# Performance work log

Measured on AMD Instinct MI355X. Metric: run time of the kernel, lower is better.

## Reference

```python
import jax, jax.numpy as jnp
import numpy as np

H, DH, BS, NSEL, WIN = 16, 64, 4, 4, 32  # heads, dim_head, compress/selection block, top-k blocks, sliding window


def rmsnorm(x):
    return x * jax.lax.rsqrt(jnp.mean(x * x, axis=-1, keepdims=True) + 1e-6)


def rope(x):
    # x: [B,S,H,d]; standard rotate-half RoPE, theta=10000
    B, S, Hh, d = x.shape
    half = d // 2
    inv = 1.0 / (10000.0 ** (jnp.arange(half, dtype=jnp.float32) / half))
    t = jnp.arange(S, dtype=jnp.float32)[:, None] * inv[None, :]
    cos = jnp.cos(t)[None, :, None, :]
    sin = jnp.sin(t)[None, :, None, :]
    x1, x2 = x[..., :half], x[..., half:]
    return jnp.concatenate([x1 * cos - x2 * sin, x1 * sin + x2 * cos], axis=-1)


def setup_inputs() -> dict:
    key = jax.random.key(0)
    ks = jax.random.split(key, 20)
    B, S, D = 2, 1024, 1024
    s = 0.02
    f32 = jnp.float32
    return {
        'x': jax.random.normal(ks[0], (B, S, D), f32),
        've': jax.random.normal(ks[1], (B, S, D), f32),
        'x0': jax.random.normal(ks[2], (B, S, D), f32),
        'lambdas': jnp.array([1.0, 0.0], f32),
        'Wq': jax.random.normal(ks[3], (D, H * DH), f32) * s,
        'Wk': jax.random.normal(ks[4], (D, H * DH), f32) * s,
        'Wv': jax.random.normal(ks[5], (D, H * DH), f32) * s,
        'pos_k': jax.random.normal(ks[6], (H, BS, DH), f32) * s,
        'pos_v': jax.random.normal(ks[7], (H, BS, DH), f32) * s,
        'Wck': jax.random.normal(ks[8], (BS * DH, DH), f32) * s,
        'Wcv': jax.random.normal(ks[9], (BS * DH, DH), f32) * s,
        'mem_k': jax.random.normal(ks[10], (H, 1, DH), f32) * s,
        'mem_v': jax.random.normal(ks[11], (H, 1, DH), f32) * s,
        'Wg': jax.random.normal(ks[12], (D, 3 * H), f32) * s,
        'Wo': jax.random.normal(ks[13], (H * DH, D), f32) * s,
        'Wfc': jax.random.normal(ks[14], (D, 4 * D), f32) * s,
        'Wproj': jax.random.normal(ks[15], (4 * D, D), f32) * s,
    }


def nsa_block(x, ve, x0, lambdas, Wq, Wk, Wv, pos_k, pos_v, Wck, Wcv, mem_k, mem_v, Wg, Wo, Wfc, Wproj):
    B, S, D = x.shape
    nB = S // BS
    scale = DH ** -0.5
    pos = jnp.arange(S)

    # lambda residual blend + rmsnorm (ve unused by NSA block)
    xr = lambdas[0] * x + lambdas[1] * x0
    h = rmsnorm(xr)

    q = (h @ Wq).reshape(B, S, H, DH)
    k = (h @ Wk).reshape(B, S, H, DH)
    v = (h @ Wv).reshape(B, S, H, DH)

    # ---- compressed-block branch ----
    kb = k.reshape(B, nB, BS, H, DH) + pos_k.transpose(1, 0, 2)[None, None]
    vb = v.reshape(B, nB, BS, H, DH) + pos_v.transpose(1, 0, 2)[None, None]
    kc = kb.transpose(0, 1, 3, 2, 4).reshape(B, nB, H, BS * DH) @ Wck  # [B,nB,H,d]
    vc = vb.transpose(0, 1, 3, 2, 4).reshape(B, nB, H, BS * DH) @ Wcv
    kc = jnp.concatenate([jnp.broadcast_to(mem_k.transpose(1, 0, 2)[None], (B, 1, H, DH)), kc], axis=1)
    vc = jnp.concatenate([jnp.broadcast_to(mem_v.transpose(1, 0, 2)[None], (B, 1, H, DH)), vc], axis=1)
    cs = jnp.einsum('bshd,bnhd->bhsn', q, kc) * scale
    block_last = jnp.arange(nB) * BS + (BS - 1)
    cvis = jnp.concatenate([jnp.ones((S, 1), bool), block_last[None, :] <= pos[:, None]], axis=1)
    cp = jax.nn.softmax(jnp.where(cvis[None, None], cs, -jnp.inf), axis=-1)
    cout = jnp.einsum('bhsn,bnhd->bshd', cp, vc)

    # ---- fine selected-block branch (top-k blocks by compressed attn mass + own diagonal block) ----
    imp = cp[..., 1:]  # [B,H,S,nB], zero for blocks not fully in the past
    sel_val, sel_idx = jax.lax.top_k(imp, NSEL)
    own = jnp.broadcast_to((pos // BS)[None, None, :, None], (B, H, S, 1)).astype(sel_idx.dtype)
    idx_all = jnp.concatenate([sel_idx, own], axis=-1)  # [B,H,S,NSEL+1]

    qr, kr = rope(q), rope(k)
    krb = kr.reshape(B, nB, BS, H, DH).transpose(0, 3, 1, 2, 4)  # [B,H,nB,Bs,d]
    vrb = v.reshape(B, nB, BS, H, DH).transpose(0, 3, 1, 2, 4)
    M = NSEL + 1
    idxf = idx_all.reshape(B, H, S * M, 1, 1)
    gk = jnp.take_along_axis(krb, idxf, axis=2).reshape(B, H, S, M * BS, DH)
    gv = jnp.take_along_axis(vrb, idxf, axis=2).reshape(B, H, S, M * BS, DH)
    kpos = idx_all[..., None] * BS + jnp.arange(BS)  # [B,H,S,M,Bs]
    vblock = jnp.concatenate([sel_val > 0, jnp.ones((B, H, S, 1), bool)], axis=-1)
    fmask = (vblock[..., None] & (kpos <= pos[None, None, :, None, None])).reshape(B, H, S, M * BS)
    fs = jnp.einsum('bshd,bhsmd->bhsm', qr, gk) * scale
    fp = jax.nn.softmax(jnp.where(fmask, fs, -jnp.inf), axis=-1)
    fout = jnp.einsum('bhsm,bhsmd->bshd', fp, gv)

    # ---- sliding-window branch ----
    off = jnp.arange(WIN)
    spos = pos[:, None] - off[None, :]  # [S,W]
    idx_s = jnp.clip(spos, 0, S - 1)
    ks_ = kr[:, idx_s]  # [B,S,W,H,d]
    vs_ = v[:, idx_s]
    ss = jnp.einsum('bshd,bswhd->bhsw', qr, ks_) * scale
    sp = jax.nn.softmax(jnp.where((spos >= 0)[None, None], ss, -jnp.inf), axis=-1)
    sout = jnp.einsum('bhsw,bswhd->bshd', sp, vs_)

    # ---- gated combine + out proj + MLP (relu^2) ----
    g = jax.nn.sigmoid(h @ Wg).reshape(B, S, H, 3)
    o = g[..., 0:1] * cout + g[..., 1:2] * fout + g[..., 2:3] * sout
    x1 = xr + o.reshape(B, S, H * DH) @ Wo
    m = rmsnorm(x1)
    return x1 + (jax.nn.relu(m @ Wfc) ** 2) @ Wproj


def reference(x, ve, x0, lambdas, Wq, Wk, Wv, pos_k, pos_v, Wck, Wcv, mem_k, mem_v, Wg, Wo, Wfc, Wproj):
    return nsa_block(x, ve, x0, lambdas, Wq, Wk, Wv, pos_k, pos_v, Wck, Wcv, mem_k, mem_v, Wg, Wo, Wfc, Wproj)
```

## Files before the change

### kernel.cpp

```cpp
#include <hip/hip_runtime.h>

constexpr int cH = 16, cDH = 64, cBS = 4, cNSEL = 4, cWIN = 32;
constexpr int cB = 2, cS = 1024, cD = 1024;
constexpr int cNB = 256, cNBLK = 257, cDFF = 4096, cM = 2048;
constexpr float cSCALE = 0.125f;
constexpr int cSSTR = 258;
constexpr int cNP = 288;

typedef unsigned short u16;
typedef unsigned int u32;
typedef __attribute__((ext_vector_type(8))) __bf16 bf16x8;
typedef __attribute__((ext_vector_type(8))) u16 u16x8;
typedef __attribute__((ext_vector_type(4))) float f32x4;
static_assert(sizeof(bf16x8) == 16, "bf16x8 must be 16B");

__device__ __forceinline__ float sigf(float x) { return 1.f / (1.f + expf(-x)); }
__device__ __forceinline__ float b2f(u16 u) {
  union { float f; u32 u; } c; c.u = ((u32)u) << 16; return c.f;
}
__device__ __forceinline__ u16 f2b(float f) {
  union { float f; u32 u; } c; c.f = f;
  u32 u = c.u;
  return (u16)((u + 0x7fffu + ((u >> 16) & 1u)) >> 16);
}
__device__ __forceinline__ void split_bf(float v, u16& h, u16& l) {
  h = f2b(v);
  l = f2b(v - b2f(h));
}

typedef const __attribute__((address_space(1))) void* gas_t;
typedef __attribute__((address_space(3))) void* las_t;
__device__ __forceinline__ void gload16(void* lds, const void* g) {
  __builtin_amdgcn_global_load_lds((gas_t)g, (las_t)lds, 16, 0, 0);
}

__global__ __launch_bounds__(256) void k_fill(float* __restrict__ p, float v)
{
  p[blockIdx.x * 256 + threadIdx.x] = v;
}

__global__ __launch_bounds__(256) void k_lerp_rmsnorm(
    const float* __restrict__ x, const float* __restrict__ x0,
    const float* __restrict__ lambdas, float* __restrict__ xr, float* __restrict__ h,
    u16* __restrict__ hbh, u16* __restrict__ hbl)
{
  int row = blockIdx.x, tid = threadIdx.x;
  float l0 = lambdas[0], l1 = lambdas[1];
  size_t base = (size_t)row * cD + tid * 4;
  float4 xa = *(const float4*)(x + base);
  float4 xb = *(const float4*)(x0 + base);
  float v0 = l0 * xa.x + l1 * xb.x;
  float v1 = l0 * xa.y + l1 * xb.y;
  float v2 = l0 * xa.z + l1 * xb.z;
  float v3 = l0 * xa.w + l1 * xb.w;
  float ss = v0*v0 + v1*v1 + v2*v2 + v3*v3;
  #pragma unroll
  for (int o = 32; o; o >>= 1) ss += __shfl_xor(ss, o);
  __shared__ float red[4];
  if ((tid & 63) == 0) red[tid >> 6] = ss;
  __syncthreads();
  float tot = red[0] + red[1] + red[2] + red[3];
  float sc = rsqrtf(tot * (1.0f / cD) + 1e-6f);
  *(float4*)(xr + base) = make_float4(v0, v1, v2, v3);
  float h0 = v0*sc, h1 = v1*sc, h2 = v2*sc, h3 = v3*sc;
  *(float4*)(h + base) = make_float4(h0, h1, h2, h3);
  if (hbh) {
    ushort4 hv, lv;
    split_bf(h0, hv.x, lv.x); split_bf(h1, hv.y, lv.y);
    split_bf(h2, hv.z, lv.z); split_bf(h3, hv.w, lv.w);
    *(ushort4*)(hbh + base) = hv;
    *(ushort4*)(hbl + base) = lv;
  }
}

__global__ __launch_bounds__(256) void k_rmsnorm(
    const float* __restrict__ x, float* __restrict__ out,
    u16* __restrict__ obh, u16* __restrict__ obl)
{
  int row = blockIdx.x, tid = threadIdx.x;
  size_t base = (size_t)row * cD + tid * 4;
  float4 v = *(const float4*)(x + base);
  float ss = v.x*v.x + v.y*v.y + v.z*v.z + v.w*v.w;
  #pragma unroll
  for (int o = 32; o; o >>= 1) ss += __shfl_xor(ss, o);
  __shared__ float red[4];
  if ((tid & 63) == 0) red[tid >> 6] = ss;
  __syncthreads();
  float tot = red[0] + red[1] + red[2] + red[3];
  float sc = rsqrtf(tot * (1.0f / cD) + 1e-6f);
  float h0 = v.x*sc, h1 = v.y*sc, h2 = v.z*sc, h3 = v.w*sc;
  if (out) *(float4*)(out + base) = make_float4(h0, h1, h2, h3);
  if (obh) {
    ushort4 hv, lv;
    split_bf(h0, hv.x, lv.x); split_bf(h1, hv.y, lv.y);
    split_bf(h2, hv.z, lv.z); split_bf(h3, hv.w, lv.w);
    *(ushort4*)(obh + base) = hv;
    *(ushort4*)(obl + base) = lv;
  }
}

template<int EPI>
__global__ __launch_bounds__(256) void k_gemm(
    const float* __restrict__ A, const float* __restrict__ Bw,
    const float* __restrict__ R, float* __restrict__ C, int M, int N, int K)
{
  constexpr int BM = 64, BN = 64, BK = 16;
  __shared__ float As[BK][BM];
  __shared__ float Bs[BK][BN];
  int tid = threadIdx.x;
  int tx = tid & 15, ty = tid >> 4;
  int m0 = blockIdx.y * BM, n0 = blockIdx.x * BN;
  float acc[4][4] = {};
  for (int k0 = 0; k0 < K; k0 += BK) {
    {
      int r = tid >> 2, c4 = (tid & 3) << 2;
      float4 av = *(const float4*)(A + (size_t)(m0 + r) * K + k0 + c4);
      As[c4+0][r] = av.x; As[c4+1][r] = av.y; As[c4+2][r] = av.z; As[c4+3][r] = av.w;
    }
    {
      int kr = tid >> 4, c4 = (tid & 15) << 2;
      int n = n0 + c4;
      const float* bp = Bw + (size_t)(k0 + kr) * N;
      if (n + 3 < N) {
        float4 bv = *(const float4*)(bp + n);
        Bs[kr][c4+0] = bv.x; Bs[kr][c4+1] = bv.y; Bs[kr][c4+2] = bv.z; Bs[kr][c4+3] = bv.w;
      } else {
        #pragma unroll
        for (int j = 0; j < 4; j++) Bs[kr][c4+j] = (n + j < N) ? bp[n + j] : 0.f;
      }
    }
    __syncthreads();
    #pragma unroll
    for (int kk = 0; kk < BK; ++kk) {
      float4 a4 = *(const float4*)&As[kk][ty << 2];
      float4 b4 = *(const float4*)&Bs[kk][tx << 2];
      float av[4] = {a4.x, a4.y, a4.z, a4.w};
      float bv[4] = {b4.x, b4.y, b4.z, b4.w};
      #pragma unroll
      for (int i = 0; i < 4; i++)
        #pragma unroll
        for (int j = 0; j < 4; j++) acc[i][j] += av[i] * bv[j];
    }
    __syncthreads();
  }
  #pragma unroll
  for (int i = 0; i < 4; i++) {
    int m = m0 + (ty << 2) + i;
    #pragma unroll
    for (int j = 0; j < 4; j++) {
      int n = n0 + (tx << 2) + j;
      if (n < N) {
        float vv = acc[i][j];
        if (EPI == 1) vv = vv > 0.f ? vv * vv : 0.f;
        if (R) vv += R[(size_t)m * N + n];
        C[(size_t)m * N + n] = vv;
      }
    }
  }
}

__global__ __launch_bounds__(256) void k_wsplit_t(
    const float* __restrict__ W, u16* __restrict__ Th, u16* __restrict__ Tl, int K, int N)
{
  __shared__ float tile[32][33];
  int n0 = blockIdx.x * 32, k0 = blockIdx.y * 32;
  int r = threadIdx.x >> 3, c4 = (threadIdx.x & 7) << 2;
  float4 v = *(const float4*)(W + (size_t)(k0 + r) * N + n0 + c4);
  tile[r][c4+0] = v.x; tile[r][c4+1] = v.y; tile[r][c4+2] = v.z; tile[r][c4+3] = v.w;
  __syncthreads();
  float f0 = tile[c4+0][r], f1 = tile[c4+1][r], f2 = tile[c4+2][r], f3 = tile[c4+3][r];
  ushort4 hv, lv;
  split_bf(f0, hv.x, lv.x); split_bf(f1, hv.y, lv.y);
  split_bf(f2, hv.z, lv.z); split_bf(f3, hv.w, lv.w);
  size_t ob = (size_t)(n0 + r) * K + k0 + c4;
  *(ushort4*)(Th + ob) = hv;
  *(ushort4*)(Tl + ob) = lv;
}

__global__ __launch_bounds__(256) void k_wsplit_g(
    const float* __restrict__ W, u16* __restrict__ Th, u16* __restrict__ Tl)
{
  int idx = blockIdx.x * 256 + threadIdx.x;
  int n = idx >> 10, kk = idx & 1023;
  float v = (n < 48) ? W[(size_t)kk * 48 + n] : 0.f;
  u16 hb, lb; split_bf(v, hb, lb);
  Th[idx] = hb; Tl[idx] = lb;
}

template<int BM, int BN, int EPI, int OUTBF, int TERMS>
__global__ __launch_bounds__(256) void k_mfma_gemm(
    const u16* __restrict__ Ah_g, const u16* __restrict__ Al_g,
    const u16* __restrict__ Bh_g, const u16* __restrict__ Bl_g,
    const float* __restrict__ R, float* __restrict__ Cf,
    u16* __restrict__ Ch, u16* __restrict__ Cl,
    int M, int N, int K)
{
  constexpr int BK = 64;
  constexpr int MR = BM / 32, NR = BN / 32;
  __shared__ u16 lds[(BM + BN) * BK * 2];
  u16* Ah = lds;
  u16* Al = Ah + BM * BK;
  u16* Bh = Al + BM * BK;
  u16* Bl = Bh + BN * BK;

  int tid = threadIdx.x;
  int lane = tid & 63, wave = tid >> 6;
  int wr = wave >> 1, wc = wave & 1;
  int l16 = lane & 15, rg = lane >> 4;

  int nwg = gridDim.x * gridDim.y;
  int lin = blockIdx.y * gridDim.x + blockIdx.x;
  if ((nwg & 7) == 0) lin = (lin & 7) * (nwg >> 3) + (lin >> 3);
  int m0 = (lin / gridDim.x) * BM, n0 = (lin % gridDim.x) * BN;

  f32x4 acc[MR][NR];
  #pragma unroll
  for (int m = 0; m < MR; m++)
    #pragma unroll
    for (int n = 0; n < NR; n++) acc[m][n] = (f32x4){0.f, 0.f, 0.f, 0.f};

  for (int k0 = 0; k0 < K; k0 += BK) {
    #pragma unroll
    for (int c = tid; c < BM * 8; c += 256) {
      int row = c >> 3, gs = (c & 7) ^ (row & 7);
      size_t off = (size_t)(m0 + row) * K + k0 + (gs << 3);
      gload16(Ah + c * 8, Ah_g + off);
      gload16(Al + c * 8, Al_g + off);
    }
    #pragma unroll
    for (int c = tid; c < BN * 8; c += 256) {
      int row = c >> 3, gs = (c & 7) ^ (row & 7);
      size_t off = (size_t)(n0 + row) * K + k0 + (gs << 3);
      gload16(Bh + c * 8, Bh_g + off);
      gload16(Bl + c * 8, Bl_g + off);
    }
    __syncthreads();

    #pragma unroll
    for (int ks = 0; ks < 2; ks++) {
      bf16x8 ah[MR], al[MR];
      #pragma unroll
      for (int m = 0; m < MR; m++) {
        int r = wr * (BM / 2) + m * 16 + l16;
        int sl = ((ks << 2) + rg) ^ (r & 7);
        ah[m] = *(const bf16x8*)&Ah[r * BK + (sl << 3)];
        al[m] = *(const bf16x8*)&Al[r * BK + (sl << 3)];
      }
      #pragma unroll
      for (int n = 0; n < NR; n++) {
        int r = wc * (BN / 2) + n * 16 + l16;
        int sl = ((ks << 2) + rg) ^ (r & 7);
        bf16x8 bh = *(const bf16x8*)&Bh[r * BK + (sl << 3)];
        bf16x8 bl = *(const bf16x8*)&Bl[r * BK + (sl << 3)];
        #pragma unroll
        for (int m = 0; m < MR; m++) {
          acc[m][n] = __builtin_amdgcn_mfma_f32_16x16x32_bf16(ah[m], bh, acc[m][n], 0, 0, 0);
          acc[m][n] = __builtin_amdgcn_mfma_f32_16x16x32_bf16(ah[m], bl, acc[m][n], 0, 0, 0);
          acc[m][n] = __builtin_amdgcn_mfma_f32_16x16x32_bf16(al[m], bh, acc[m][n], 0, 0, 0);
          if (TERMS == 4)
            acc[m][n] = __builtin_amdgcn_mfma_f32_16x16x32_bf16(al[m], bl, acc[m][n], 0, 0, 0);
        }
      }
    }
    __syncthreads();
  }

  int rbase = m0 + wr * (BM / 2) + (rg << 2);
  #pragma unroll
  for (int m = 0; m < MR; m++) {
    #pragma unroll
    for (int j = 0; j < 4; j++) {
      int row = rbase + m * 16 + j;
      #pragma unroll
      for (int n = 0; n < NR; n++) {
        int col = n0 + wc * (BN / 2) + n * 16 + l16;
        float v = acc[m][n][j];
        if (EPI == 1) v = v > 0.f ? v * v : 0.f;
        if (R) v += R[(size_t)row * N + col];
        if (OUTBF != 1) Cf[(size_t)row * N + col] = v;
        if (OUTBF >= 1) {
          u16 hb, lb; split_bf(v, hb, lb);
          Ch[(size_t)row * N + col] = hb;
          Cl[(size_t)row * N + col] = lb;
        }
      }
    }
  }
}

__global__ __launch_bounds__(256) void k_mfma_qkvg(
    const u16* __restrict__ Ahg, const u16* __restrict__ Alg,
    const u16* __restrict__ BqH, const u16* __restrict__ BqL,
    const u16* __restrict__ BkH, const u16* __restrict__ BkL,
    const u16* __restrict__ BvH, const u16* __restrict__ BvL,
    const u16* __restrict__ BgH, const u16* __restrict__ BgL,
    float* __restrict__ qo, float* __restrict__ ko, float* __restrict__ vo,
    float* __restrict__ gpre, u16* __restrict__ qbh, u16* __restrict__ qbl)
{
  constexpr int BM = 64, BN = 64, BK = 64, K = cD;
  __shared__ u16 lds[(BM + BN) * BK * 2];
  u16* Ah = lds;
  u16* Al = Ah + BM * BK;
  u16* Bh = Al + BM * BK;
  u16* Bl = Bh + BN * BK;

  int tid = threadIdx.x;
  int lane = tid & 63, wave = tid >> 6;
  int wr = wave >> 1, wc = wave & 1;
  int l16 = lane & 15, rg = lane >> 4;

  int nwg = gridDim.x * gridDim.y;
  int lin = blockIdx.y * gridDim.x + blockIdx.x;
  lin = (lin & 7) * (nwg >> 3) + (lin >> 3);
  int bx = lin % gridDim.x, by = lin / gridDim.x;
  int mat = bx >> 4;
  int n0 = (bx - (mat << 4)) * BN;
  int m0 = by * BM;

  const u16* Bh_g; const u16* Bl_g;
  if (mat == 0)      { Bh_g = BqH; Bl_g = BqL; }
  else if (mat == 1) { Bh_g = BkH; Bl_g = BkL; }
  else if (mat == 2) { Bh_g = BvH; Bl_g = BvL; }
  else               { Bh_g = BgH; Bl_g = BgL; }

  f32x4 acc[2][2];
  #pragma unroll
  for (int m = 0; m < 2; m++)
    #pragma unroll
    for (int n = 0; n < 2; n++) acc[m][n] = (f32x4){0.f, 0.f, 0.f, 0.f};

  for (int k0 = 0; k0 < K; k0 += BK) {
    #pragma unroll
    for (int c = tid; c < BM * 8; c += 256) {
      int row = c >> 3, gs = (c & 7) ^ (row & 7);
      size_t off = (size_t)(m0 + row) * K + k0 + (gs << 3);
      gload16(Ah + c * 8, Ahg + off);
      gload16(Al + c * 8, Alg + off);
    }
    #pragma unroll
    for (int c = tid; c < BN * 8; c += 256) {
      int row = c >> 3, gs = (c & 7) ^ (row & 7);
      size_t off = (size_t)(n0 + row) * K + k0 + (gs << 3);
      gload16(Bh + c * 8, Bh_g + off);
      gload16(Bl + c * 8, Bl_g + off);
    }
    __syncthreads();

    #pragma unroll
    for (int ks = 0; ks < 2; ks++) {
      bf16x8 ah[2], al[2];
      #pragma unroll
      for (int m = 0; m < 2; m++) {
        int r = wr * 32 + m * 16 + l16;
        int sl = ((ks << 2) + rg) ^ (r & 7);
        ah[m] = *(const bf16x8*)&Ah[r * BK + (sl << 3)];
        al[m] = *(const bf16x8*)&Al[r * BK + (sl << 3)];
      }
      #pragma unroll
      for (int n = 0; n < 2; n++) {
        int r = wc * 32 + n * 16 + l16;
        int sl = ((ks << 2) + rg) ^ (r & 7);
        bf16x8 bh = *(const bf16x8*)&Bh[r * BK + (sl << 3)];
        bf16x8 bl = *(const bf16x8*)&Bl[r * BK + (sl << 3)];
        #pragma unroll
        for (int m = 0; m < 2; m++) {
          acc[m][n] = __builtin_amdgcn_mfma_f32_16x16x32_bf16(ah[m], bh, acc[m][n], 0, 0, 0);
          acc[m][n] = __builtin_amdgcn_mfma_f32_16x16x32_bf16(ah[m], bl, acc[m][n], 0, 0, 0);
          acc[m][n] = __builtin_amdgcn_mfma_f32_16x16x32_bf16(al[m], bh, acc[m][n], 0, 0, 0);
          acc[m][n] = __builtin_amdgcn_mfma_f32_16x16x32_bf16(al[m], bl, acc[m][n], 0, 0, 0);
        }
      }
    }
    __syncthreads();
  }

  int rbase = m0 + wr * 32 + (rg << 2);
  #pragma unroll
  for (int m = 0; m < 2; m++) {
    #pragma unroll
    for (int j = 0; j < 4; j++) {
      int row = rbase + m * 16 + j;
      #pragma unroll
      for (int n = 0; n < 2; n++) {
        int col = n0 + wc * 32 + n * 16 + l16;
        float v = acc[m][n][j];
        if (mat == 0) {
          qo[(size_t)row * cD + col] = v;
          u16 hb, lb; split_bf(v, hb, lb);
          qbh[(size_t)row * cD + col] = hb;
          qbl[(size_t)row * cD + col] = lb;
        } else if (mat == 1) {
          ko[(size_t)row * cD + col] = v;
        } else if (mat == 2) {
          vo[(size_t)row * cD + col] = v;
        } else if (col < 48) {
          gpre[(size_t)row * 48 + col] = v;
        }
      }
    }
  }
}

__global__ __launch_bounds__(64) void k_compress4(
    const float* __restrict__ kbuf, const float* __restrict__ vbuf,
    const float* __restrict__ pos_k, const float* __restrict__ pos_v,
    const float* __restrict__ Wck, const float* __restrict__ Wcv,
    const float* __restrict__ mem_k, const float* __restrict__ mem_v,
    float* __restrict__ kc, float* __restrict__ vc)
{
  int idx = blockIdx.x;
  int h = idx % cH; int n = (idx / cH) % cNBLK; int b = idx / (cH * cNBLK);
  int d = threadIdx.x;
  size_t co = (((size_t)b * cNBLK + n) * cH + h) * cDH + d;
  if (n == 0) {
    kc[co] = mem_k[h * cDH + d];
    vc[co] = mem_v[h * cDH + d];
    return;
  }
  __shared__ float kb[cBS * cDH], vb[cBS * cDH];
  int nb = n - 1;
  for (int t = d; t < cBS * cDH; t += 64) {
    int i = t >> 6, e = t & 63;
    size_t src = (((size_t)b * cS + nb * cBS + i) * cH + h) * cDH + e;
    kb[t] = kbuf[src] + pos_k[(h * cBS + i) * cDH + e];
    vb[t] = vbuf[src] + pos_v[(h * cBS + i) * cDH + e];
  }
  __syncthreads();
  float ak = 0.f, av = 0.f;
  #pragma unroll 4
  for (int j = 0; j < cBS * cDH; ++j) {
    ak += kb[j] * Wck[(size_t)j * cDH + d];
    av += vb[j] * Wcv[(size_t)j * cDH + d];
  }
  kc[co] = ak; vc[co] = av;
}

__global__ __launch_bounds__(256) void k_compress4_bf(
    const float* __restrict__ kbuf, const float* __restrict__ vbuf,
    const float* __restrict__ pos_k, const float* __restrict__ pos_v,
    const float* __restrict__ Wck, const float* __restrict__ Wcv,
    const float* __restrict__ mem_k, const float* __restrict__ mem_v,
    u16* __restrict__ kch, u16* __restrict__ kcl,
    u16* __restrict__ vth, u16* __restrict__ vtl)
{
  int wave = threadIdx.x >> 6, d = threadIdx.x & 63;
  int idx = blockIdx.x * 4 + wave;
  int h = idx % cH;
  int n = (idx / cH) % cNBLK;
  int b = idx / (cH * cNBLK);
  float ak, av;
  if (n == 0) {
    ak = mem_k[h * cDH + d];
    av = mem_v[h * cDH + d];
    size_t vr = ((size_t)(b * cH + h) * cDH + d) * cNP;
    for (int p = cNBLK; p < cNP; p++) { vth[vr + p] = 0; vtl[vr + p] = 0; }
  } else {
    __shared__ float kb[4][cBS * cDH], vb[4][cBS * cDH];
    int nb = n - 1;
    for (int t = d; t < cBS * cDH; t += 64) {
      int i = t >> 6, e = t & 63;
      size_t src = (((size_t)b * cS + nb * cBS + i) * cH + h) * cDH + e;
      kb[wave][t] = kbuf[src] + pos_k[(h * cBS + i) * cDH + e];
      vb[wave][t] = vbuf[src] + pos_v[(h * cBS + i) * cDH + e];
    }
    __syncthreads();
    ak = 0.f; av = 0.f;
    #pragma unroll 4
    for (int j = 0; j < cBS * cDH; ++j) {
      ak += kb[wave][j] * Wck[(size_t)j * cDH + d];
      av += vb[wave][j] * Wcv[(size_t)j * cDH + d];
    }
  }
  u16 kh, kl, vh, vl;
  split_bf(ak, kh, kl); split_bf(av, vh, vl);
  size_t kco = ((size_t)(b * cH + h) * cNP + n) * cDH + d;
  kch[kco] = kh; kcl[kco] = kl;
  size_t vco = ((size_t)(b * cH + h) * cDH + d) * cNP + n;
  vth[vco] = vh; vtl[vco] = vl;
}

__device__ __forceinline__ void top4_insert(float sv, int bi,
    float& v0, float& v1, float& v2, float& v3, int& i0, int& i1, int& i2, int& i3)
{
  if (sv > v3) {
    if (sv > v0)      { v3=v2;i3=i2; v2=v1;i2=i1; v1=v0;i1=i0; v0=sv;i0=bi; }
    else if (sv > v1) { v3=v2;i3=i2; v2=v1;i2=i1; v1=sv;i1=bi; }
    else if (sv > v2) { v3=v2;i3=i2; v2=sv;i2=bi; }
    else              { v3=sv;i3=bi; }
  }
}

__device__ __forceinline__ void top4_ins_tie(float sv, int bi,
    float& v0, float& v1, float& v2, float& v3, int& i0, int& i1, int& i2, int& i3)
{
  bool b3 = (sv > v3) || (sv == v3 && bi < i3);
  if (!b3) return;
  bool b0 = (sv > v0) || (sv == v0 && bi < i0);
  bool b1 = (sv > v1) || (sv == v1 && bi < i1);
  bool b2 = (sv > v2) || (sv == v2 && bi < i2);
  if (b0)      { v3=v2;i3=i2; v2=v1;i2=i1; v1=v0;i1=i0; v0=sv;i0=bi; }
  else if (b1) { v3=v2;i3=i2; v2=v1;i2=i1; v1=sv;i1=bi; }
  else if (b2) { v3=v2;i3=i2; v2=sv;i2=bi; }
  else         { v3=sv;i3=bi; }
}

template<int CNT>
__device__ __forceinline__ void cattn_cols(
    int base, int lane, int s_row, const float* __restrict__ kcb,
    const float* __restrict__ qrow, u16* __restrict__ ssb, float& lm,
    float& v0, float& v1, float& v2, float& v3,
    int& i0, int& i1, int& i2, int& i3)
{
  float sreg[CNT];
  #pragma unroll
  for (int u = 0; u < CNT; u++) sreg[u] = 0.f;
  #pragma unroll
  for (int d0 = 0; d0 < 4; d0++) {
    float4 qc0 = ((const float4*)qrow)[d0 * 4 + 0];
    float4 qc1 = ((const float4*)qrow)[d0 * 4 + 1];
    float4 qc2 = ((const float4*)qrow)[d0 * 4 + 2];
    float4 qc3 = ((const float4*)qrow)[d0 * 4 + 3];
    #pragma unroll
    for (int u = 0; u < CNT; u++) {
      int n = base + u;
      if (n < cNBLK) {
        const float4* kp = (const float4*)(kcb + (size_t)n * (cH * cDH) + d0 * 16);
        float4 k0 = kp[0], k1 = kp[1], k2 = kp[2], k3 = kp[3];
        sreg[u] += qc0.x*k0.x + qc0.y*k0.y + qc0.z*k0.z + qc0.w*k0.w
                 + qc1.x*k1.x + qc1.y*k1.y + qc1.z*k1.z + qc1.w*k1.w
                 + qc2.x*k2.x + qc2.y*k2.y + qc2.z*k2.z + qc2.w*k2.w
                 + qc3.x*k3.x + qc3.y*k3.y + qc3.z*k3.z + qc3.w*k3.w;
      }
    }
  }
  #pragma unroll
  for (int u = 0; u < CNT; u++) {
    int n = base + u;
    if (n >= cNBLK) continue;
    float a = sreg[u] * cSCALE;
    bool vis = (n == 0) || ((n - 1) * cBS + (cBS - 1) <= s_row);
    float sv = vis ? a : -INFINITY;
    ssb[lane * cSSTR + n] = f2b(sv);
    lm = fmaxf(lm, sv);
    if (n >= 1) top4_insert(sv, n - 1, v0, v1, v2, v3, i0, i1, i2, i3);
  }
}

__global__ __launch_bounds__(512, 4) void k_cattn_tile(
    const float* __restrict__ q, const float* __restrict__ kc, const float* __restrict__ vc,
    float* __restrict__ cout, float* __restrict__ sel_val, int* __restrict__ sel_idx)
{
  constexpr int NW = 8;
  constexpr int NCH = 33;
  __shared__ u16  ssb[64 * cSSTR];
  __shared__ float lmax[NW][64];
  __shared__ float lsum[NW][64];
  __shared__ float t4v[NW][64][4];
  __shared__ int   t4i[NW][64][4];
  __shared__ float mxs[64];
  __shared__ float invs[64];

  int tile = blockIdx.x & 15;
  int h = (blockIdx.x >> 4) & 15;
  int b = blockIdx.x >> 8;
  int s0 = tile * 64;
  int t = threadIdx.x;
  int lane = t & 63, wave = t >> 6;

  const float* kcb = kc + ((size_t)b * cNBLK * cH + h) * cDH;
  const float* vcb = vc + ((size_t)b * cNBLK * cH + h) * cDH;
  const int nstride = cH * cDH;

  {
    int r = lane;
    int s_row = s0 + r;
    const float* qrow = q + (((size_t)b * cS + s_row) * cH + h) * cDH;
    float v0=-INFINITY,v1=-INFINITY,v2=-INFINITY,v3=-INFINITY;
    int i0=0,i1=0,i2=0,i3=0;
    float lm = -INFINITY;
    int nb0 = wave * NCH;
    cattn_cols<11>(nb0,      r, s_row, kcb, qrow, ssb, lm, v0,v1,v2,v3, i0,i1,i2,i3);
    cattn_cols<11>(nb0 + 11, r, s_row, kcb, qrow, ssb, lm, v0,v1,v2,v3, i0,i1,i2,i3);
    cattn_cols<11>(nb0 + 22, r, s_row, kcb, qrow, ssb, lm, v0,v1,v2,v3, i0,i1,i2,i3);
    lmax[wave][lane] = lm;
    t4v[wave][lane][0]=v0; t4v[wave][lane][1]=v1; t4v[wave][lane][2]=v2; t4v[wave][lane][3]=v3;
    t4i[wave][lane][0]=i0; t4i[wave][lane][1]=i1; t4i[wave][lane][2]=i2; t4i[wave][lane][3]=i3;
  }
  __syncthreads();

  if (wave == 0) {
    int r = lane;
    float mx = -INFINITY;
    #pragma unroll
    for (int c = 0; c < NW; c++) mx = fmaxf(mx, lmax[c][r]);
    mxs[r] = mx;
    float v0=-INFINITY,v1=-INFINITY,v2=-INFINITY,v3=-INFINITY;
    int i0=0,i1=0,i2=0,i3=0;
    #pragma unroll
    for (int c = 0; c < NW; c++)
      #pragma unroll
      for (int u = 0; u < 4; u++)
        top4_insert(t4v[c][r][u], t4i[c][r][u], v0, v1, v2, v3, i0, i1, i2, i3);
    t4v[0][r][0]=v0; t4v[0][r][1]=v1; t4v[0][r][2]=v2; t4v[0][r][3]=v3;
    t4i[0][r][0]=i0; t4i[0][r][1]=i1; t4i[0][r][2]=i2; t4i[0][r][3]=i3;
  }
  __syncthreads();

  {
    int r = lane;
    float mx = mxs[r];
    float s = 0.f;
    int nb0 = wave * NCH;
    int nb1 = min(cNBLK, nb0 + NCH);
    for (int n = nb0; n < nb1; n++) {
      float sv = b2f(ssb[r * cSSTR + n]);
      float e = expf(sv - mx);
      ssb[r * cSSTR + n] = f2b(e);
      s += e;
    }
    lsum[wave][r] = s;
  }
  __syncthreads();

  if (wave == 0) {
    int r = lane;
    float sum = 0.f;
    #pragma unroll
    for (int c = 0; c < NW; c++) sum += lsum[c][r];
    float inv = 1.f / sum;
    invs[r] = inv;
    float mx = mxs[r];
    size_t so = (((size_t)b * cH + h) * cS + (s0 + r)) * cNSEL;
    #pragma unroll
    for (int u = 0; u < 4; u++) {
      sel_val[so + u] = expf(t4v[0][r][u] - mx) * inv;
      sel_idx[so + u] = t4i[0][r][u];
    }
  }
  __syncthreads();

  {
    int r = t >> 3, dq = t & 7;
    float4 a0 = {0,0,0,0}, a1 = {0,0,0,0};
    const u16* erow = ssb + r * cSSTR;
    const float* vbase = vcb + dq * 8;
#define ACC8(ee, w0, w1) \
    a0.x += (ee)*(w0).x; a0.y += (ee)*(w0).y; a0.z += (ee)*(w0).z; a0.w += (ee)*(w0).w; \
    a1.x += (ee)*(w1).x; a1.y += (ee)*(w1).y; a1.z += (ee)*(w1).z; a1.w += (ee)*(w1).w;
    for (int n = 0; n < 256; n += 4) {
      float e0 = b2f(erow[n+0]), e1 = b2f(erow[n+1]);
      float e2 = b2f(erow[n+2]), e3 = b2f(erow[n+3]);
      const float4* p0 = (const float4*)(vbase + (size_t)(n+0) * nstride);
      const float4* p1 = (const float4*)(vbase + (size_t)(n+1) * nstride);
      const float4* p2 = (const float4*)(vbase + (size_t)(n+2) * nstride);
      const float4* p3 = (const float4*)(vbase + (size_t)(n+3) * nstride);
      float4 w00 = p0[0], w01 = p0[1];
      float4 w10 = p1[0], w11 = p1[1];
      float4 w20 = p2[0], w21 = p2[1];
      float4 w30 = p3[0], w31 = p3[1];
      ACC8(e0, w00, w01)
      ACC8(e1, w10, w11)
      ACC8(e2, w20, w21)
      ACC8(e3, w30, w31)
    }
    {
      float e0 = b2f(erow[256]);
      const float4* p0 = (const float4*)(vbase + (size_t)256 * nstride);
      float4 w00 = p0[0], w01 = p0[1];
      ACC8(e0, w00, w01)
    }
#undef ACC8
    float inv = invs[r];
    float* crow = cout + (((size_t)b * cS + s0 + r) * cH + h) * cDH + dq * 8;
    ((float4*)crow)[0] = make_float4(a0.x*inv, a0.y*inv, a0.z*inv, a0.w*inv);
    ((float4*)crow)[1] = make_float4(a1.x*inv, a1.y*inv, a1.z*inv, a1.w*inv);
  }
}

__global__ __launch_bounds__(256) void k_cattn_mfma(
    const u16* __restrict__ qbh, const u16* __restrict__ qbl,
    const u16* __restrict__ kch, const u16* __restrict__ kcl,
    const u16* __restrict__ vth, const u16* __restrict__ vtl,
    float* __restrict__ cout, float* __restrict__ sel_val, int* __restrict__ sel_idx)
{
  constexpr int SSTW = 296;
  __shared__ u16 sws[4 * 16 * SSTW];

  int bid = (blockIdx.x & 7) * 64 + (blockIdx.x >> 3);
  int lane = threadIdx.x & 63, w = threadIdx.x >> 6;
  int l16 = lane & 15, rg = lane >> 4, g8 = rg << 3;
  int tile = (bid & 15) * 4 + w;
  int h = (bid >> 4) & 15, b = bid >> 8;
  int s0 = tile * 16;
  u16* sraw = sws + w * 16 * SSTW;

  size_t qrow = (((size_t)b * cS + (s0 + l16)) * cH + h) * cDH;
  bf16x8 qh0 = *(const bf16x8*)(qbh + qrow + g8);
  bf16x8 qh1 = *(const bf16x8*)(qbh + qrow + 32 + g8);
  bf16x8 ql0 = *(const bf16x8*)(qbl + qrow + g8);
  bf16x8 ql1 = *(const bf16x8*)(qbl + qrow + 32 + g8);

  const u16* kchb = kch + (size_t)(b * cH + h) * cNP * cDH;
  const u16* kclb = kcl + (size_t)(b * cH + h) * cNP * cDH;

  float v0=-INFINITY, v1=-INFINITY, v2=-INFINITY, v3=-INFINITY;
  int i0=0, i1=0, i2=0, i3=0;
  float lm = -INFINITY;

  for (int nt = 0; nt < 18; nt++) {
    size_t krow = (size_t)(nt * 16 + l16) * cDH;
    bf16x8 kh0 = *(const bf16x8*)(kchb + krow + g8);
    bf16x8 kh1 = *(const bf16x8*)(kchb + krow + 32 + g8);
    bf16x8 kl0 = *(const bf16x8*)(kclb + krow + g8);
    bf16x8 kl1 = *(const bf16x8*)(kclb + krow + 32 + g8);
    f32x4 acc = (f32x4){0.f, 0.f, 0.f, 0.f};
    acc = __builtin_amdgcn_mfma_f32_16x16x32_bf16(kh0, qh0, acc, 0, 0, 0);
    acc = __builtin_amdgcn_mfma_f32_16x16x32_bf16(kh1, qh1, acc, 0, 0, 0);
    acc = __builtin_amdgcn_mfma_f32_16x16x32_bf16(kh0, ql0, acc, 0, 0, 0);
    acc = __builtin_amdgcn_mfma_f32_16x16x32_bf16(kh1, ql1, acc, 0, 0, 0);
    acc = __builtin_amdgcn_mfma_f32_16x16x32_bf16(kl0, qh0, acc, 0, 0, 0);
    acc = __builtin_amdgcn_mfma_f32_16x16x32_bf16(kl1, qh1, acc, 0, 0, 0);
    acc = __builtin_amdgcn_mfma_f32_16x16x32_bf16(kl0, ql0, acc, 0, 0, 0);
    acc = __builtin_amdgcn_mfma_f32_16x16x32_bf16(kl1, ql1, acc, 0, 0, 0);
    u16 sb[4];
    #pragma unroll
    for (int j = 0; j < 4; j++) {
      int n = nt * 16 + rg * 4 + j;
      float a = acc[j] * cSCALE;
      bool vis = (n < cNBLK) && ((n == 0) || ((n - 1) * cBS + (cBS - 1) <= s0 + l16));
      float sv = vis ? a : -INFINITY;
      sb[j] = f2b(sv);
      lm = fmaxf(lm, sv);
      if (n >= 1) top4_ins_tie(sv, n - 1, v0, v1, v2, v3, i0, i1, i2, i3);
    }
    int cw = nt * 16 + rg * 4;
    *(u32*)&sraw[l16 * SSTW + cw]     = (u32)sb[0] | ((u32)sb[1] << 16);
    *(u32*)&sraw[l16 * SSTW + cw + 2] = (u32)sb[2] | ((u32)sb[3] << 16);
  }

  #pragma unroll
  for (int o = 16; o < 64; o <<= 1) {
    lm = fmaxf(lm, __shfl_xor(lm, o));
    float p0 = __shfl_xor(v0, o), p1 = __shfl_xor(v1, o);
    float p2 = __shfl_xor(v2, o), p3 = __shfl_xor(v3, o);
    int   q0 = __shfl_xor(i0, o), q1 = __shfl_xor(i1, o);
    int   q2 = __shfl_xor(i2, o), q3 = __shfl_xor(i3, o);
    top4_ins_tie(p0, q0, v0, v1, v2, v3, i0, i1, i2, i3);
    top4_ins_tie(p1, q1, v0, v1, v2, v3, i0, i1, i2, i3);
    top4_ins_tie(p2, q2, v0, v1, v2, v3, i0, i1, i2, i3);
    top4_ins_tie(p3, q3, v0, v1, v2, v3, i0, i1, i2, i3);
  }

  float sum = 0.f;
  for (int nt = 0; nt < 18; nt++) {
    int cw = nt * 16 + rg * 4;
    u32 w01 = *(u32*)&sraw[l16 * SSTW + cw];
    u32 w23 = *(u32*)&sraw[l16 * SSTW + cw + 2];
    float e0 = expf(b2f((u16)(w01 & 0xffff)) - lm);
    float e1 = expf(b2f((u16)(w01 >> 16)) - lm);
    float e2 = expf(b2f((u16)(w23 & 0xffff)) - lm);
    float e3 = expf(b2f((u16)(w23 >> 16)) - lm);
    sum += (e0 + e1) + (e2 + e3);
    *(u32*)&sraw[l16 * SSTW + cw]     = (u32)f2b(e0) | ((u32)f2b(e1) << 16);
    *(u32*)&sraw[l16 * SSTW + cw + 2] = (u32)f2b(e2) | ((u32)f2b(e3) << 16);
  }
  #pragma unroll
  for (int o = 16; o < 64; o <<= 1) sum += __shfl_xor(sum, o);
  float inv = 1.f / sum;

  if (rg == 0) {
    size_t so = (((size_t)b * cH + h) * cS + (s0 + l16)) * cNSEL;
    sel_val[so + 0] = expf(v0 - lm) * inv; sel_idx[so + 0] = i0;
    sel_val[so + 1] = expf(v1 - lm) * inv; sel_idx[so + 1] = i1;
    sel_val[so + 2] = expf(v2 - lm) * inv; sel_idx[so + 2] = i2;
    sel_val[so + 3] = expf(v3 - lm) * inv; sel_idx[so + 3] = i3;
  }
  __syncthreads();

  const u16* vthb = vth + (size_t)(b * cH + h) * cDH * cNP;
  const u16* vtlb = vtl + (size_t)(b * cH + h) * cDH * cNP;
  f32x4 pacc[4];
  #pragma unroll
  for (int dt = 0; dt < 4; dt++) pacc[dt] = (f32x4){0.f, 0.f, 0.f, 0.f};
  for (int kc9 = 0; kc9 < 9; kc9++) {
    bf16x8 ef = *(const bf16x8*)&sraw[l16 * SSTW + kc9 * 32 + g8];
    #pragma unroll
    for (int dt = 0; dt < 4; dt++) {
      size_t vrow = (size_t)(dt * 16 + l16) * cNP + kc9 * 32 + g8;
      bf16x8 vh = *(const bf16x8*)(vthb + vrow);
      bf16x8 vl = *(const bf16x8*)(vtlb + vrow);
      pacc[dt] = __builtin_amdgcn_mfma_f32_16x16x32_bf16(vh, ef, pacc[dt], 0, 0, 0);
      pacc[dt] = __builtin_amdgcn_mfma_f32_16x16x32_bf16(vl, ef, pacc[dt], 0, 0, 0);
    }
  }
  float* crow = cout + (((size_t)b * cS + (s0 + l16)) * cH + h) * cDH;
  #pragma unroll
  for (int dt = 0; dt < 4; dt++) {
    *(float4*)(crow + dt * 16 + rg * 4) =
        make_float4(pacc[dt][0] * inv, pacc[dt][1] * inv,
                    pacc[dt][2] * inv, pacc[dt][3] * inv);
  }
}

__global__ __launch_bounds__(256) void k_rope(float* __restrict__ q, float* __restrict__ k)
{
  int t = blockIdx.x * 256 + threadIdx.x;
  int j = t & 31; int h = (t >> 5) & (cH - 1); int bs = t >> 9;
  int s = bs & (cS - 1);
  float inv = expf(-(float)j * 0.28782313662425575f);
  float ang = (float)s * inv;
  float sn, c; sincosf(ang, &sn, &c);
  size_t base = ((size_t)bs * cH + h) * cDH;
  float q1 = q[base + j], q2 = q[base + j + 32];
  q[base + j]      = q1 * c - q2 * sn;
  q[base + j + 32] = q1 * sn + q2 * c;
  float k1 = k[base + j], k2 = k[base + j + 32];
  k[base + j]      = k1 * c - k2 * sn;
  k[base + j + 32] = k1 * sn + k2 * c;
}

__global__ __launch_bounds__(256) void k_fsattn(
    const float* __restrict__ qr, const float* __restrict__ kr, const float* __restrict__ v,
    const float* __restrict__ sel_val, const int* __restrict__ sel_idx,
    float* __restrict__ fout, float* __restrict__ sout)
{
  int wave = threadIdx.x >> 6, lane = threadIdx.x & 63;
  int sidx = blockIdx.x * 4 + wave;
  int s = sidx % cS; int h = (sidx / cS) % cH; int b = sidx / (cS * cH);
  __shared__ float qs[4][cDH];
  __shared__ float pf[4][20];
  __shared__ float ps[4][cWIN];
  __shared__ int blk[4][5];
  __shared__ int bok[4][5];
  size_t qoff = (((size_t)b * cS + s) * cH + h) * cDH;
  qs[wave][lane] = qr[qoff + lane];
  if (lane < 5) {
    size_t so = (((size_t)b * cH + h) * cS + s) * cNSEL;
    if (lane < 4) { blk[wave][lane] = sel_idx[so + lane]; bok[wave][lane] = sel_val[so + lane] > 0.f; }
    else          { blk[wave][4] = s / cBS; bok[wave][4] = 1; }
  }
  __syncthreads();

  const float* kp = nullptr;
  if (lane < 20) {
    int tt = lane >> 2, i = lane & 3;
    int kpos = blk[wave][tt] * cBS + i;
    if (bok[wave][tt] && kpos <= s)
      kp = kr + (((size_t)b * cS + kpos) * cH + h) * cDH;
  } else if (lane >= 32) {
    int sp = s - (lane - 32);
    if (sp >= 0)
      kp = kr + (((size_t)b * cS + sp) * cH + h) * cDH;
  }
  float sc = -INFINITY;
  if (kp) {
    float a = 0.f;
    #pragma unroll 16
    for (int e = 0; e < cDH; e++) a += qs[wave][e] * kp[e];
    sc = a * cSCALE;
  }
  float mx = sc;
  #pragma unroll
  for (int o = 16; o; o >>= 1) mx = fmaxf(mx, __shfl_xor(mx, o, 32));
  float ex = (sc == -INFINITY) ? 0.f : expf(sc - mx);
  float sum = ex;
  #pragma unroll
  for (int o = 16; o; o >>= 1) sum += __shfl_xor(sum, o, 32);
  float pp = ex / sum;
  if (lane < 20) pf[wave][lane] = pp;
  if (lane >= 32) ps[wave][lane - 32] = pp;
  __syncthreads();

  float accf = 0.f;
  for (int tt = 0; tt < 5; tt++) {
    if (!bok[wave][tt]) continue;
    int kbase = blk[wave][tt] * cBS;
    #pragma unroll
    for (int i = 0; i < cBS; i++) {
      float pm = pf[wave][tt * cBS + i];
      if (pm != 0.f)
        accf += pm * v[(((size_t)b * cS + kbase + i) * cH + h) * cDH + lane];
    }
  }
  float accs = 0.f;
  int wm = min(cWIN, s + 1);
  for (int w = 0; w < wm; w++)
    accs += ps[wave][w] * v[(((size_t)b * cS + s - w) * cH + h) * cDH + lane];
  fout[qoff + lane] = accf;
  sout[qoff + lane] = accs;
}

__global__ __launch_bounds__(256) void k_combine(
    const float* __restrict__ gpre, const float* __restrict__ cout,
    const float* __restrict__ fout, const float* __restrict__ sout, float* __restrict__ o)
{
  int t = blockIdx.x * 256 + threadIdx.x;
  int hh = (t >> 6) & 15; int bs = t >> 10;
  float g0 = sigf(gpre[(size_t)bs * 48 + hh * 3 + 0]);
  float g1 = sigf(gpre[(size_t)bs * 48 + hh * 3 + 1]);
  float g2 = sigf(gpre[(size_t)bs * 48 + hh * 3 + 2]);
  o[t] = g0 * cout[t] + g1 * fout[t] + g2 * sout[t];
}

__global__ __launch_bounds__(256) void k_combine_bf(
    const float* __restrict__ gpre, const float* __restrict__ cout,
    const float* __restrict__ fout, const float* __restrict__ sout,
    u16* __restrict__ oh, u16* __restrict__ ol)
{
  int t = blockIdx.x * 256 + threadIdx.x;
  int hh = (t >> 6) & 15; int bs = t >> 10;
  float g0 = sigf(gpre[(size_t)bs * 48 + hh * 3 + 0]);
  float g1 = sigf(gpre[(size_t)bs * 48 + hh * 3 + 1]);
  float g2 = sigf(gpre[(size_t)bs * 48 + hh * 3 + 2]);
  float v = g0 * cout[t] + g1 * fout[t] + g2 * sout[t];
  u16 hb, lb; split_bf(v, hb, lb);
  oh[t] = hb; ol[t] = lb;
}

extern "C" void kernel_launch(void* const* d_in, const int* in_sizes, int n_in,
                              void* d_out, int out_size, void* d_ws, size_t ws_size,
                              hipStream_t stream) {
  float* out = (float*)d_out;

  static const int exp_sizes[17] = {
    2097152, 2097152, 2097152, 2,
    1048576, 1048576, 1048576,
    4096, 4096,
    16384, 16384,
    1024, 1024,
    49152, 1048576, 4194304, 4194304
  };
  if (n_in < 17) {
    k_fill<<<dim3(8192), dim3(256), 0, stream>>>(out, 500.0f + 10.0f * n_in);
    return;
  }
  for (int i = 0; i < 17; ++i) {
    if (in_sizes[i] != exp_sizes[i] && in_sizes[i] != 4 * exp_sizes[i]) {
      k_fill<<<dim3(8192), dim3(256), 0, stream>>>(out, 1000.0f + 50.0f * i);
      return;
    }
  }

  const float* x     = (const float*)d_in[0];
  const float* x0    = (const float*)d_in[2];
  const float* lam   = (const float*)d_in[3];
  const float* Wq    = (const float*)d_in[4];
  const float* Wk    = (const float*)d_in[5];
  const float* Wv    = (const float*)d_in[6];
  const float* pos_k = (const float*)d_in[7];
  const float* pos_v = (const float*)d_in[8];
  const float* Wck   = (const float*)d_in[9];
  const float* Wcv   = (const float*)d_in[10];
  const float* mem_k = (const float*)d_in[11];
  const float* mem_v = (const float*)d_in[12];
  const float* Wg    = (const float*)d_in[13];
  const float* Wo    = (const float*)d_in[14];
  const float* Wfc   = (const float*)d_in[15];
  const float* Wpr   = (const float*)d_in[16];

  float* ws = (float*)d_ws;
  const size_t E = (size_t)cM * cD;
  float* gpre = ws;
  float* selv = ws + 98304;
  int*   seli = (int*)(ws + 98304 + 131072);
  u16* WgTh = (u16*)(ws + 360448);
  u16* WgTl = WgTh + 65536;
  const size_t A0 = 1048576;
  float* xr = ws + A0 + 0 * E;
  float* h  = ws + A0 + 1 * E;
  float* q  = ws + A0 + 2 * E;
  float* k  = ws + A0 + 3 * E;
  float* v  = ws + A0 + 4 * E;
  float* co = ws + A0 + 5 * E;
  float* fo = ws + A0 + 6 * E;
  float* so = ws + A0 + 7 * E;
  float* x1 = ws + A0 + 8 * E;
  float* fc = ws + A0 + 2 * E;
  float* kc = fo;
  float* vc = so;

  const size_t P = A0 + 9 * E;
  const size_t NEED_FLOATS = P + 14680064;
  bool use_mfma = (ws_size >= NEED_FLOATS * sizeof(float));

  u16* WvTh = (u16*)(ws + P);              u16* WvTl = WvTh + 1048576;
  u16* WoTh = (u16*)(ws + P + 1048576);    u16* WoTl = WoTh + 1048576;
  u16* WfcTh = (u16*)(ws + P + 2097152);   u16* WfcTl = WfcTh + 4194304;
  u16* WprTh = (u16*)(ws + P + 6291456);   u16* WprTl = WprTh + 4194304;
  u16* hbh = (u16*)(ws + P + 10485760);    u16* hbl = hbh + 2097152;
  u16* obh = (u16*)(ws + P + 12582912);    u16* obl = obh + 2097152;
  u16* mbh = (u16*)h;                      u16* mbl = mbh + 2097152;
  u16* fbh = (u16*)q;                      u16* fbl = fbh + 8388608;
  u16* WqTh = (u16*)x1;                    u16* WqTl = WqTh + 1048576;
  u16* WkTh = WqTh + 2097152;              u16* WkTl = WqTh + 3145728;
  const size_t KCN = (size_t)cB * cH * cNP * cDH;
  u16* kch = (u16*)fo;       u16* kcl = kch + KCN;
  u16* vth = kcl + KCN;      u16* vtl = vth + KCN;
  u16* qbh = (u16*)so;       u16* qbl = qbh + 2097152;

  dim3 b256(256), b64(64), b512(512);
  dim3 gSq(cD / 64, cM / 64);

  if (use_mfma) {
    k_wsplit_t<<<dim3(32, 32), b256, 0, stream>>>(Wq, WqTh, WqTl, 1024, 1024);
    k_wsplit_t<<<dim3(32, 32), b256, 0, stream>>>(Wk, WkTh, WkTl, 1024, 1024);
    k_wsplit_t<<<dim3(32, 32), b256, 0, stream>>>(Wv, WvTh, WvTl, 1024, 1024);
    k_wsplit_t<<<dim3(32, 32), b256, 0, stream>>>(Wo, WoTh, WoTl, 1024, 1024);
    k_wsplit_t<<<dim3(128, 32), b256, 0, stream>>>(Wfc, WfcTh, WfcTl, 1024, 4096);
    k_wsplit_t<<<dim3(32, 128), b256, 0, stream>>>(Wpr, WprTh, WprTl, 4096, 1024);
    k_wsplit_g<<<dim3(256), b256, 0, stream>>>(Wg, WgTh, WgTl);

    k_lerp_rmsnorm<<<dim3(cM), b256, 0, stream>>>(x, x0, lam, xr, h, hbh, hbl);

    k_mfma_qkvg<<<dim3(49, 32), b256, 0, stream>>>(
        hbh, hbl, WqTh, WqTl, WkTh, WkTl, WvTh, WvTl, WgTh, WgTl,
        q, k, v, gpre, qbh, qbl);

    k_compress4_bf<<<dim3(cB * cNBLK * cH / 4), b256, 0, stream>>>(
        k, v, pos_k, pos_v, Wck, Wcv, mem_k, mem_v, kch, kcl, vth, vtl);
    k_cattn_mfma<<<dim3(cB * cH * 16), b256, 0, stream>>>(
        qbh, qbl, kch, kcl, vth, vtl, co, selv, seli);
    k_rope<<<dim3(cB * cS * cH * 32 / 256), b256, 0, stream>>>(q, k);
    k_fsattn<<<dim3(cB * cH * cS / 4), b256, 0, stream>>>(q, k, v, selv, seli, fo, so);

    k_combine_bf<<<dim3((cM * cD) / 256), b256, 0, stream>>>(gpre, co, fo, so, obh, obl);

    k_mfma_gemm<64, 64, 0, 0, 3><<<dim3(cD / 64, cM / 64), b256, 0, stream>>>(
        obh, obl, WoTh, WoTl, xr, x1, nullptr, nullptr, cM, cD, cD);

    k_rmsnorm<<<dim3(cM), b256, 0, stream>>>(x1, nullptr, mbh, mbl);

    k_mfma_gemm<64, 128, 1, 1, 3><<<dim3(cDFF / 128, cM / 64), b256, 0, stream>>>(
        mbh, mbl, WfcTh, WfcTl, nullptr, nullptr, fbh, fbl, cM, cDFF, cD);

    k_mfma_gemm<64, 64, 0, 0, 3><<<dim3(cD / 64, cM / 64), b256, 0, stream>>>(
        fbh, fbl, WprTh, WprTl, x1, out, nullptr, nullptr, cM, cD, cDFF);
  } else {
    k_lerp_rmsnorm<<<dim3(cM), b256, 0, stream>>>(x, x0, lam, xr, h, nullptr, nullptr);
    k_gemm<0><<<gSq, b256, 0, stream>>>(h, Wq, nullptr, q, cM, cD, cD);
    k_gemm<0><<<gSq, b256, 0, stream>>>(h, Wk, nullptr, k, cM, cD, cD);
    k_gemm<0><<<gSq, b256, 0, stream>>>(h, Wv, nullptr, v, cM, cD, cD);
    k_gemm<0><<<dim3(1, cM / 64), b256, 0, stream>>>(h, Wg, nullptr, gpre, cM, 48, cD);
    k_compress4<<<dim3(cB * cNBLK * cH), b64, 0, stream>>>(k, v, pos_k, pos_v, Wck, Wcv,
                                                           mem_k, mem_v, kc, vc);
    k_cattn_tile<<<dim3(cB * cH * 16), b512, 0, stream>>>(q, kc, vc, co, selv, seli);
    k_rope<<<dim3(cB * cS * cH * 32 / 256), b256, 0, stream>>>(q, k);
    k_fsattn<<<dim3(cB * cH * cS / 4), b256, 0, stream>>>(q, k, v, selv, seli, fo, so);
    k_combine<<<dim3((cM * cD) / 256), b256, 0, stream>>>(gpre, co, fo, so, co);
    k_gemm<0><<<gSq, b256, 0, stream>>>(co, Wo, xr, x1, cM, cD, cD);
    k_rmsnorm<<<dim3(cM), b256, 0, stream>>>(x1, h, nullptr, nullptr);
    k_gemm<1><<<dim3(cDFF / 64, cM / 64), b256, 0, stream>>>(h, Wfc, nullptr, fc, cM, cDFF, cD);
    k_gemm<0><<<gSq, b256, 0, stream>>>(fc, Wpr, x1, out, cM, cD, cDFF);
  }
}
```

Baseline: 626.3 us.

## Stage compressed K and V tiles in shared memory for compressed attention

Compressed keys (hi/lo bf16 split) and transposed values are loaded cooperatively into an LDS buffer, using an XOR swizzle for K, in halves. All four waves of a block, which share the same (b,h), then read from LDS instead of each issuing its own global loads. This removes redundant global/L2 traffic across the waves, at the cost of about 40KB extra LDS per block, which lowers occupancy, and of added barriers. It relies on gload16, which must be defined elsewhere, and it affects only one of several kernels.

```diff
diff --git a/kernel.cpp b/kernel.cpp
--- a/kernel.cpp
+++ b/kernel.cpp
@@ -684,10 +684,12 @@
     float* __restrict__ cout, float* __restrict__ sel_val, int* __restrict__ sel_idx)
 {
   constexpr int SSTW = 296;
+  __shared__ u16 kbuf[20480];
   __shared__ u16 sws[4 * 16 * SSTW];
 
+  int tid = threadIdx.x;
   int bid = (blockIdx.x & 7) * 64 + (blockIdx.x >> 3);
-  int lane = threadIdx.x & 63, w = threadIdx.x >> 6;
+  int lane = tid & 63, w = tid >> 6;
   int l16 = lane & 15, rg = lane >> 4, g8 = rg << 3;
   int tile = (bid & 15) * 4 + w;
   int h = (bid >> 4) & 15, b = bid >> 8;
@@ -702,40 +704,65 @@
 
   const u16* kchb = kch + (size_t)(b * cH + h) * cNP * cDH;
   const u16* kclb = kcl + (size_t)(b * cH + h) * cNP * cDH;
+  const u16* vthb = vth + (size_t)(b * cH + h) * cDH * cNP;
+  const u16* vtlb = vtl + (size_t)(b * cH + h) * cDH * cNP;
 
   float v0=-INFINITY, v1=-INFINITY, v2=-INFINITY, v3=-INFINITY;
   int i0=0, i1=0, i2=0, i3=0;
   float lm = -INFINITY;
 
-  for (int nt = 0; nt < 18; nt++) {
-    size_t krow = (size_t)(nt * 16 + l16) * cDH;
-    bf16x8 kh0 = *(const bf16x8*)(kchb + krow + g8);
-    bf16x8 kh1 = *(const bf16x8*)(kchb + krow + 32 + g8);
-    bf16x8 kl0 = *(const bf16x8*)(kclb + krow + g8);
-    bf16x8 kl1 = *(const bf16x8*)(kclb + krow + 32 + g8);
-    f32x4 acc = (f32x4){0.f, 0.f, 0.f, 0.f};
-    acc = __builtin_amdgcn_mfma_f32_16x16x32_bf16(kh0, qh0, acc, 0, 0, 0);
-    acc = __builtin_amdgcn_mfma_f32_16x16x32_bf16(kh1, qh1, acc, 0, 0, 0);
-    acc = __builtin_amdgcn_mfma_f32_16x16x32_bf16(kh0, ql0, acc, 0, 0, 0);
-    acc = __builtin_amdgcn_mfma_f32_16x16x32_bf16(kh1, ql1, acc, 0, 0, 0);
-    acc = __builtin_amdgcn_mfma_f32_16x16x32_bf16(kl0, qh0, acc, 0, 0, 0);
-    acc = __builtin_amdgcn_mfma_f32_16x16x32_bf16(kl1, qh1, acc, 0, 0, 0);
-    acc = __builtin_amdgcn_mfma_f32_16x16x32_bf16(kl0, ql0, acc, 0, 0, 0);
-    acc = __builtin_amdgcn_mfma_f32_16x16x32_bf16(kl1, ql1, acc, 0, 0, 0);
-    u16 sb[4];
-    #pragma unroll
-    for (int j = 0; j < 4; j++) {
-      int n = nt * 16 + rg * 4 + j;
-      float a = acc[j] * cSCALE;
-      bool vis = (n < cNBLK) && ((n == 0) || ((n - 1) * cBS + (cBS - 1) <= s0 + l16));
-      float sv = vis ? a : -INFINITY;
-      sb[j] = f2b(sv);
-      lm = fmaxf(lm, sv);
-      if (n >= 1) top4_ins_tie(sv, n - 1, v0, v1, v2, v3, i0, i1, i2, i3);
-    }
-    int cw = nt * 16 + rg * 4;
-    *(u32*)&sraw[l16 * SSTW + cw]     = (u32)sb[0] | ((u32)sb[1] << 16);
-    *(u32*)&sraw[l16 * SSTW + cw + 2] = (u32)sb[2] | ((u32)sb[3] << 16);
+  #pragma unroll
+  for (int half = 0; half < 2; half++) {
+    for (int c = tid; c < 2304; c += 256) {
+      int rr = c >> 3, G = (c & 7) ^ (rr & 7);
+      const u16* src = (rr < 144)
+          ? kchb + (size_t)(half * 144 + rr) * cDH + (G << 3)
+          : kclb + (size_t)(half * 144 + rr - 144) * cDH + (G << 3);
+      gload16(kbuf + c * 8, src);
+    }
+    __syncthreads();
+    for (int ntl = 0; ntl < 9; ntl++) {
+      int nt = half * 9 + ntl;
+      int r = ntl * 16 + l16;
+      int sw0 = ((rg ^ (r & 7)) << 3);
+      int sw1 = (((rg + 4) ^ (r & 7)) << 3);
+      bf16x8 kh0 = *(const bf16x8*)&kbuf[r * 64 + sw0];
+      bf16x8 kh1 = *(const bf16x8*)&kbuf[r * 64 + sw1];
+      bf16x8 kl0 = *(const bf16x8*)&kbuf[(144 + r) * 64 + sw0];
+      bf16x8 kl1 = *(const bf16x8*)&kbuf[(144 + r) * 64 + sw1];
+      f32x4 acc = (f32x4){0.f, 0.f, 0.f, 0.f};
+      acc = __builtin_amdgcn_mfma_f32_16x16x32_bf16(kh0, qh0, acc, 0, 0, 0);
+      acc = __builtin_amdgcn_mfma_f32_16x16x32_bf16(kh1, qh1, acc, 0, 0, 0);
+      acc = __builtin_amdgcn_mfma_f32_16x16x32_bf16(kh0, ql0, acc, 0, 0, 0);
+      acc = __builtin_amdgcn_mfma_f32_16x16x32_bf16(kh1, ql1, acc, 0, 0, 0);
+      acc = __builtin_amdgcn_mfma_f32_16x16x32_bf16(kl0, qh0, acc, 0, 0, 0);
+      acc = __builtin_amdgcn_mfma_f32_16x16x32_bf16(kl1, qh1, acc, 0, 0, 0);
+      acc = __builtin_amdgcn_mfma_f32_16x16x32_bf16(kl0, ql0, acc, 0, 0, 0);
+      acc = __builtin_amdgcn_mfma_f32_16x16x32_bf16(kl1, ql1, acc, 0, 0, 0);
+      u16 sb[4];
+      #pragma unroll
+      for (int j = 0; j < 4; j++) {
+        int n = nt * 16 + rg * 4 + j;
+        float a = acc[j] * cSCALE;
+        bool vis = (n < cNBLK) && ((n == 0) || ((n - 1) * cBS + (cBS - 1) <= s0 + l16));
+        float sv = vis ? a : -INFINITY;
+        sb[j] = f2b(sv);
+        lm = fmaxf(lm, sv);
+        if (n >= 1) top4_ins_tie(sv, n - 1, v0, v1, v2, v3, i0, i1, i2, i3);
+      }
+      int cw = nt * 16 + rg * 4;
+      *(u32*)&sraw[l16 * SSTW + cw]     = (u32)sb[0] | ((u32)sb[1] << 16);
+      *(u32*)&sraw[l16 * SSTW + cw + 2] = (u32)sb[2] | ((u32)sb[3] << 16);
+    }
+    __syncthreads();
+  }
+
+  for (int c = tid; c < 2560; c += 256) {
+    int ngr = c >> 7, drow = c & 127;
+    const u16* src = (drow < 64)
+        ? vthb + (size_t)drow * cNP + (ngr << 3)
+        : vtlb + (size_t)(drow - 64) * cNP + (ngr << 3);
+    gload16(kbuf + c * 8, src);
   }
 
   #pragma unroll
@@ -777,18 +804,36 @@
   }
   __syncthreads();
 
-  const u16* vthb = vth + (size_t)(b * cH + h) * cDH * cNP;
-  const u16* vtlb = vtl + (size_t)(b * cH + h) * cDH * cNP;
   f32x4 pacc[4];
   #pragma unroll
   for (int dt = 0; dt < 4; dt++) pacc[dt] = (f32x4){0.f, 0.f, 0.f, 0.f};
-  for (int kc9 = 0; kc9 < 9; kc9++) {
+  for (int kc9 = 0; kc9 < 5; kc9++) {
     bf16x8 ef = *(const bf16x8*)&sraw[l16 * SSTW + kc9 * 32 + g8];
+    int ngr = kc9 * 4 + rg;
     #pragma unroll
     for (int dt = 0; dt < 4; dt++) {
-      size_t vrow = (size_t)(dt * 16 + l16) * cNP + kc9 * 32 + g8;
-      bf16x8 vh = *(const bf16x8*)(vthb + vrow);
-      bf16x8 vl = *(const bf16x8*)(vtlb + vrow);
+      bf16x8 vh = *(const bf16x8*)&kbuf[(ngr * 128 + dt * 16 + l16) * 8];
+      bf16x8 vl = *(const bf16x8*)&kbuf[(ngr * 128 + 64 + dt * 16 + l16) * 8];
+      pacc[dt] = __builtin_amdgcn_mfma_f32_16x16x32_bf16(vh, ef, pacc[dt], 0, 0, 0);
+      pacc[dt] = __builtin_amdgcn_mfma_f32_16x16x32_bf16(vl, ef, pacc[dt], 0, 0, 0);
+    }
+  }
+  __syncthreads();
+  for (int c = tid; c < 2048; c += 256) {
+    int ngr = c >> 7, drow = c & 127;
+    const u16* src = (drow < 64)
+        ? vthb + (size_t)drow * cNP + 160 + (ngr << 3)
+        : vtlb + (size_t)(drow - 64) * cNP + 160 + (ngr << 3);
+    gload16(kbuf + c * 8, src);
+  }
+  __syncthreads();
+  for (int kc9 = 5; kc9 < 9; kc9++) {
+    bf16x8 ef = *(const bf16x8*)&sraw[l16 * SSTW + kc9 * 32 + g8];
+    int ngr = (kc9 - 5) * 4 + rg;
+    #pragma unroll
+    for (int dt = 0; dt < 4; dt++) {
+      bf16x8 vh = *(const bf16x8*)&kbuf[(ngr * 128 + dt * 16 + l16) * 8];
+      bf16x8 vl = *(const bf16x8*)&kbuf[(ngr * 128 + 64 + dt * 16 + l16) * 8];
       pacc[dt] = __builtin_amdgcn_mfma_f32_16x16x32_bf16(vh, ef, pacc[dt], 0, 0, 0);
       pacc[dt] = __builtin_amdgcn_mfma_f32_16x16x32_bf16(vl, ef, pacc[dt], 0, 0, 0);
     }
```

Result: no change. 632.9 us (+1.0%).
